# Kernel tuning notes

Measured on AMD Instinct MI355X. Metric: run time of the kernel, lower is better.

Reference implementation:

```python
import jax, jax.numpy as jnp
import numpy as np

# ASPPConv constants (from init_kwargs)
K = 9                      # kernel_size
DILATION = 6
PAD = DILATION * (K // 2)  # 24, 'same' padding for dilated conv
SIGMA = DILATION * 1.0     # self.sigma = dilation * sigma
BN_EPS = 1e-5


def setup_inputs() -> dict:
    key = jax.random.key(0)
    k1, k2, k3 = jax.random.split(key, 3)
    B, C, O, L = 8, 256, 16384, 0  # placeholder to keep names readable
    B, Cin, Cout, L = 8, 256, 256, 16384
    x = jax.random.normal(k1, (B, Cin, L), dtype=jnp.float32)
    coords = jax.random.uniform(k2, (B, 3, L), dtype=jnp.float32)  # xyz per point
    weight = jax.random.normal(k3, (Cout, Cin, K), dtype=jnp.float32) * 0.05
    gamma = jnp.ones((Cout,), jnp.float32)
    beta = jnp.zeros((Cout,), jnp.float32)
    return {"x": x, "coords": coords, "weight": weight, "gamma": gamma, "beta": beta}


def _weighted_conv1d(x, coords, weight):
    """Dilated conv1d where each tap is scaled by a Gaussian of the squared
    euclidean distance between the tap's coordinates and the center point's
    coordinates: w_k = exp(-||c_k - c_center||^2 / (2*sigma^2)).
    Zero padding (matches F.unfold) for both x and coords."""
    B, C, L = x.shape
    x_pad = jnp.pad(x, ((0, 0), (0, 0), (PAD, PAD)))
    c_pad = jnp.pad(coords, ((0, 0), (0, 0), (PAD, PAD)))
    inv_2s2 = 1.0 / (2.0 * SIGMA * SIGMA)
    out = jnp.zeros((B, weight.shape[0], L), x.dtype)
    # K=9 taps: small fixed loop; avoids materializing the [B,C,K,L] unfold.
    for k in range(K):
        off = k * DILATION
        xk = jax.lax.dynamic_slice_in_dim(x_pad, off, L, axis=2)   # [B,C,L]
        ck = jax.lax.dynamic_slice_in_dim(c_pad, off, L, axis=2)   # [B,3,L]
        dist2 = jnp.sum((ck - coords) ** 2, axis=1)                # [B,L]
        wk = jnp.exp(-dist2 * inv_2s2)                             # [B,L]
        out = out + jnp.einsum('bcl,oc->bol', xk * wk[:, None, :], weight[:, :, k])
    return out


def reference(x, coords, weight, gamma, beta):
    y = _weighted_conv1d(x, coords, weight)                        # [B,O,L]
    # BatchNorm1d (training mode): stats over batch and length per channel
    mean = jnp.mean(y, axis=(0, 2), keepdims=True)
    var = jnp.var(y, axis=(0, 2), keepdims=True)
    y = (y - mean) * jax.lax.rsqrt(var + BN_EPS)
    y = y * gamma[None, :, None] + beta[None, :, None]
    return jax.nn.relu(y)
```

## Files before the change

### kernel.cpp

```cpp
#include <hip/hip_runtime.h>
#include <hip/hip_bf16.h>

#define LEN   16384
#define CIN   256
#define COUT  256
#define NB    8
#define NTAP  9
#define DIL   6
#define PADW  24
#define NSTEP 72
#define PADROWS (LEN + 2*PADW)

typedef __bf16 bf16x8 __attribute__((ext_vector_type(8)));
typedef float  f32x4  __attribute__((ext_vector_type(4)));
typedef unsigned short u16;
typedef u16 u16x8 __attribute__((ext_vector_type(8)));

#define WKT_BYTES  (NB*NTAP*LEN*4)
#define WB_BYTES   (NSTEP*256*32*2)
#define XT_OFF     (WKT_BYTES + WB_BYTES)
#define XT_BYTES   ((size_t)NB*PADROWS*256*2)
#define SUMS_OFF   (XT_OFF + XT_BYTES)
#define SCB_OFF    (SUMS_OFF + 512*4)

#define GLOAD_LDS(g, l) __builtin_amdgcn_global_load_lds( \
    (const __attribute__((address_space(1))) void*)(g),   \
    (__attribute__((address_space(3))) void*)(l), 16, 0, 0)

__device__ __forceinline__ u16 f2bf(float v) {
    unsigned u = __builtin_bit_cast(unsigned, v);
    u += 0x7FFFu + ((u >> 16) & 1u);
    return (u16)(u >> 16);
}

__global__ __launch_bounds__(256) void k_wk(const float* __restrict__ coords,
                                            float* __restrict__ wkt) {
    int i = blockIdx.x * 256 + threadIdx.x;
    if (i >= NB * NTAP * LEN) return;
    int l = i & (LEN - 1);
    int bk = i >> 14;
    int k = bk % NTAP, b = bk / NTAP;
    const float* cb = coords + (size_t)b * 3 * LEN;
    int lt = l + k * DIL - PADW;
    bool ok = (unsigned)lt < (unsigned)LEN;
    float d2 = 0.f;
#pragma unroll
    for (int j = 0; j < 3; ++j) {
        float cc = cb[j * LEN + l];
        float ct = ok ? cb[j * LEN + lt] : 0.f;
        float d = ct - cc;
        d2 += d * d;
    }
    wkt[i] = expf(-d2 * (1.f / 72.f));
}

__global__ __launch_bounds__(256) void k_wb(const float* __restrict__ W,
                                            u16* __restrict__ Wb) {
    int i = blockIdx.x * 256 + threadIdx.x;
    if (i >= NSTEP * 256 * 32) return;
    int j = i & 31;
    int o = (i >> 5) & 255;
    int s = i >> 13;
    int k = s >> 3;
    int c = ((s & 7) << 5) + j;
    Wb[i] = f2bf(W[((size_t)o * CIN + c) * NTAP + k]);
}

__global__ __launch_bounds__(256) void k_xt(const float* __restrict__ x,
                                            u16* __restrict__ xt) {
    __shared__ float t[64 * 65];
    const int tid = threadIdx.x;
    const int cg  = blockIdx.x;
    const int rg  = blockIdx.y;
    const int b   = blockIdx.z;
    const int lx0 = rg * 64 - PADW;
#pragma unroll
    for (int i = 0; i < 4; ++i) {
        int c  = i * 16 + (tid >> 4);
        int l4 = (tid & 15) * 4;
        int lx = lx0 + l4;
        f32x4 v = {};
        if (lx >= 0 && lx + 3 < LEN)
            v = *reinterpret_cast<const f32x4*>(
                x + ((size_t)b * CIN + cg * 64 + c) * LEN + lx);
        float* tr = &t[c * 65 + l4];
        tr[0] = v[0]; tr[1] = v[1]; tr[2] = v[2]; tr[3] = v[3];
    }
    __syncthreads();
#pragma unroll
    for (int m = 0; m < 2; ++m) {
        int l    = m * 32 + (tid >> 3);
        int c0   = (tid & 7) * 8;
        int prow = rg * 64 + l;
        if (prow < PADROWS) {
            u16x8 o;
#pragma unroll
            for (int j = 0; j < 8; ++j) o[j] = f2bf(t[(c0 + j) * 65 + l]);
            *reinterpret_cast<u16x8*>(
                xt + ((size_t)b * PADROWS + prow) * 256 + cg * 64 + c0) = o;
        }
    }
}

__global__ __launch_bounds__(256, 2) void k_conv(
    const u16*   __restrict__ xt,
    const float* __restrict__ wkt,
    const u16*   __restrict__ Wb,
    float* __restrict__ y,
    float* __restrict__ sums)
{
    const int lt = blockIdx.x;
    const int ob = blockIdx.y;
    const int b  = blockIdx.z;
    const int l0 = lt * 128;
    const int tid  = threadIdx.x;
    const int lane = tid & 63;
    const int wid  = tid >> 6;
    const int wr = wid >> 1;
    const int wc = wid & 1;

    __shared__ u16 As[3][4096];
    __shared__ u16 Bs[3][4096];
    __shared__ float wkl[NTAP * 128];

    for (int i = tid; i < NTAP * 128; i += 256) {
        int k = i >> 7, l = i & 127;
        wkl[i] = wkt[((size_t)b * NTAP + k) * LEN + l0 + l];
    }

    f32x4 acc_f[4][4] = {};
    f32x4 acc_t[4][4] = {};

    const u16* wbBase = Wb + (size_t)ob * 4096;
    const u16* xtBase = xt + (size_t)b * PADROWS * 256;
    const int srcswz = ((lane & 3) ^ ((lane >> 3) & 3)) * 8;
    const int rsub   = lane >> 2;

    auto stage = [&](int bufi, int s) {
        const int ktap  = s >> 3;
        const int cbase = (s & 7) << 5;
#pragma unroll
        for (int j = 0; j < 2; ++j) {
            const int q = wid * 2 + j;
            const u16* ga = wbBase + (size_t)s * 8192 + (q * 16 + rsub) * 32 + srcswz;
            GLOAD_LDS(ga, &As[bufi][q * 512]);
            const u16* gb = xtBase
                + (size_t)(l0 + q * 16 + rsub + 6 * ktap) * 256
                + cbase + srcswz;
            GLOAD_LDS(gb, &Bs[bufi][q * 512]);
        }
    };

    stage(0, 0);
    stage(1, 1);
    __syncthreads();

    const int fr  = lane & 15;
    const int rdoff = fr * 32 + (((lane >> 4) ^ ((fr >> 1) & 3)) * 8);
    const int col = lane & 15;
    const int rg  = lane >> 4;

    for (int s = 0; s < NSTEP; ++s) {
        const int cur = s % 3;
        asm volatile("s_waitcnt vmcnt(4)" ::: "memory");
        __builtin_amdgcn_s_barrier();
        if (s + 2 < NSTEP) stage((s + 2) % 3, s + 2);

        bf16x8 af[4], bfv[4];
        const u16* Ab = &As[cur][wr * 2048 + rdoff];
        const u16* Bb = &Bs[cur][wc * 2048 + rdoff];
#pragma unroll
        for (int mi = 0; mi < 4; ++mi)
            af[mi] = *reinterpret_cast<const bf16x8*>(Ab + mi * 512);
#pragma unroll
        for (int ni = 0; ni < 4; ++ni)
            bfv[ni] = *reinterpret_cast<const bf16x8*>(Bb + ni * 512);
#pragma unroll
        for (int mi = 0; mi < 4; ++mi)
#pragma unroll
            for (int ni = 0; ni < 4; ++ni)
                acc_t[mi][ni] = __builtin_amdgcn_mfma_f32_16x16x32_bf16(
                    af[mi], bfv[ni], acc_t[mi][ni], 0, 0, 0);
        if ((s & 7) == 7) {
            const int ktap = s >> 3;
            float wv[4];
#pragma unroll
            for (int ni = 0; ni < 4; ++ni)
                wv[ni] = wkl[ktap * 128 + wc * 64 + ni * 16 + col];
#pragma unroll
            for (int mi = 0; mi < 4; ++mi)
#pragma unroll
                for (int ni = 0; ni < 4; ++ni) {
#pragma unroll
                    for (int r = 0; r < 4; ++r)
                        acc_f[mi][ni][r] += wv[ni] * acc_t[mi][ni][r];
                    acc_t[mi][ni] = f32x4{};
                }
        }
    }

    float* yb = y + ((size_t)b * COUT + ob * 128 + wr * 64) * LEN + l0 + wc * 64;
#pragma unroll
    for (int mi = 0; mi < 4; ++mi) {
#pragma unroll
        for (int r = 0; r < 4; ++r) {
            const int o_loc = mi * 16 + rg * 4 + r;
            float s1 = 0.f, s2 = 0.f;
#pragma unroll
            for (int ni = 0; ni < 4; ++ni) {
                float v = acc_f[mi][ni][r];
                yb[(size_t)o_loc * LEN + ni * 16 + col] = v;
                s1 += v;
                s2 += v * v;
            }
#pragma unroll
            for (int m = 1; m < 16; m <<= 1) {
                s1 += __shfl_xor(s1, m, 64);
                s2 += __shfl_xor(s2, m, 64);
            }
            if (col == 0) {
                int o = ob * 128 + wr * 64 + o_loc;
                atomicAdd(&sums[o], s1);
                atomicAdd(&sums[COUT + o], s2);
            }
        }
    }
}

__global__ __launch_bounds__(256) void k_stats(const float* __restrict__ sums,
                                               const float* __restrict__ gamma,
                                               const float* __restrict__ beta,
                                               float* __restrict__ scb) {
    int o = threadIdx.x;
    const float inv_n = 1.f / (float)(NB * LEN);
    float mean = sums[o] * inv_n;
    float var  = sums[COUT + o] * inv_n - mean * mean;
    float sc = gamma[o] * rsqrtf(var + 1e-5f);
    scb[o]        = sc;
    scb[COUT + o] = beta[o] - mean * sc;
}

__global__ __launch_bounds__(256) void k_norm(float* __restrict__ y,
                                              const float* __restrict__ scb) {
    const int total4 = NB * COUT * LEN / 4;
    int i = blockIdx.x * 256 + threadIdx.x;
    for (; i < total4; i += gridDim.x * 256) {
        f32x4 v = reinterpret_cast<f32x4*>(y)[i];
        int o = (i >> 12) & 255;
        float sc = scb[o], bi = scb[COUT + o];
#pragma unroll
        for (int j = 0; j < 4; ++j)
            v[j] = fmaxf(v[j] * sc + bi, 0.f);
        reinterpret_cast<f32x4*>(y)[i] = v;
    }
}

extern "C" void kernel_launch(void* const* d_in, const int* in_sizes, int n_in,
                              void* d_out, int out_size, void* d_ws, size_t ws_size,
                              hipStream_t stream) {
    const float* x      = (const float*)d_in[0];
    const float* coords = (const float*)d_in[1];
    const float* W      = (const float*)d_in[2];
    const float* gamma  = (const float*)d_in[3];
    const float* beta   = (const float*)d_in[4];
    float* out = (float*)d_out;
    char*  ws  = (char*)d_ws;

    float* wkt  = (float*)ws;
    u16*   Wb   = (u16*)(ws + WKT_BYTES);
    u16*   xtp  = (u16*)(ws + XT_OFF);
    float* sums = (float*)(ws + SUMS_OFF);
    float* scb  = (float*)(ws + SCB_OFF);

    hipMemsetAsync(sums, 0, 512 * 4, stream);

    k_wk<<<(NB * NTAP * LEN + 255) / 256, 256, 0, stream>>>(coords, wkt);
    k_wb<<<(NSTEP * 256 * 32 + 255) / 256, 256, 0, stream>>>(W, Wb);
    k_xt<<<dim3(4, (PADROWS + 63) / 64, NB), 256, 0, stream>>>(x, xtp);

    dim3 g(LEN / 128, 2, NB);
    k_conv<<<g, 256, 0, stream>>>(xtp, wkt, Wb, out, sums);

    k_stats<<<1, 256, 0, stream>>>(sums, gamma, beta, scb);
    k_norm<<<2048, 256, 0, stream>>>(out, scb);
}
```

Baseline: 441.7 us.

## Deepen LDS pipeline to 4 buffers and double-buffer register fragments around MFMA

Moves the shared-memory ring from 3 to 4 stages with three loads in flight, and unrolls the k-loop by two. LDS fragment reads for the next step are ping-ponged into a second register set so they overlap the current step's MFMAs. MFMA blocks are wrapped in s_setprio to favour matrix issue across waves. This raises LDS use and register pressure and adds barriers, which may reduce occupancy at two blocks per CU.

```diff
diff --git a/kernel.cpp b/kernel.cpp
--- a/kernel.cpp
+++ b/kernel.cpp
@@ -119,8 +119,8 @@
     const int wr = wid >> 1;
     const int wc = wid & 1;
 
-    __shared__ u16 As[3][4096];
-    __shared__ u16 Bs[3][4096];
+    __shared__ u16 As[4][4096];
+    __shared__ u16 Bs[4][4096];
     __shared__ float wkl[NTAP * 128];
 
     for (int i = tid; i < NTAP * 128; i += 256) {
@@ -136,7 +136,8 @@
     const int srcswz = ((lane & 3) ^ ((lane >> 3) & 3)) * 8;
     const int rsub   = lane >> 2;
 
-    auto stage = [&](int bufi, int s) {
+    auto stage = [&](int s) {
+        const int bufi  = s & 3;
         const int ktap  = s >> 3;
         const int cbase = (s & 7) << 5;
 #pragma unroll
@@ -151,52 +152,74 @@
         }
     };
 
-    stage(0, 0);
-    stage(1, 1);
-    __syncthreads();
-
-    const int fr  = lane & 15;
+    const int fr    = lane & 15;
     const int rdoff = fr * 32 + (((lane >> 4) ^ ((fr >> 1) & 3)) * 8);
-    const int col = lane & 15;
-    const int rg  = lane >> 4;
-
-    for (int s = 0; s < NSTEP; ++s) {
-        const int cur = s % 3;
-        asm volatile("s_waitcnt vmcnt(4)" ::: "memory");
-        __builtin_amdgcn_s_barrier();
-        if (s + 2 < NSTEP) stage((s + 2) % 3, s + 2);
-
-        bf16x8 af[4], bfv[4];
-        const u16* Ab = &As[cur][wr * 2048 + rdoff];
-        const u16* Bb = &Bs[cur][wc * 2048 + rdoff];
+    const int col   = lane & 15;
+    const int rg    = lane >> 4;
+
+    auto readf = [&](bf16x8* af, bf16x8* bfv, int s) {
+        const u16* Ab = &As[s & 3][wr * 2048 + rdoff];
+        const u16* Bb = &Bs[s & 3][wc * 2048 + rdoff];
 #pragma unroll
         for (int mi = 0; mi < 4; ++mi)
             af[mi] = *reinterpret_cast<const bf16x8*>(Ab + mi * 512);
 #pragma unroll
         for (int ni = 0; ni < 4; ++ni)
             bfv[ni] = *reinterpret_cast<const bf16x8*>(Bb + ni * 512);
+    };
+
+    auto domfma = [&](bf16x8* af, bf16x8* bfv) {
+        __builtin_amdgcn_s_setprio(1);
 #pragma unroll
         for (int mi = 0; mi < 4; ++mi)
 #pragma unroll
             for (int ni = 0; ni < 4; ++ni)
                 acc_t[mi][ni] = __builtin_amdgcn_mfma_f32_16x16x32_bf16(
                     af[mi], bfv[ni], acc_t[mi][ni], 0, 0, 0);
-        if ((s & 7) == 7) {
-            const int ktap = s >> 3;
-            float wv[4];
-#pragma unroll
-            for (int ni = 0; ni < 4; ++ni)
-                wv[ni] = wkl[ktap * 128 + wc * 64 + ni * 16 + col];
-#pragma unroll
-            for (int mi = 0; mi < 4; ++mi)
-#pragma unroll
-                for (int ni = 0; ni < 4; ++ni) {
-#pragma unroll
-                    for (int r = 0; r < 4; ++r)
-                        acc_f[mi][ni][r] += wv[ni] * acc_t[mi][ni][r];
-                    acc_t[mi][ni] = f32x4{};
-                }
-        }
+        __builtin_amdgcn_s_setprio(0);
+    };
+
+    auto fold = [&](int s) {
+        const int ktap = s >> 3;
+        float wv[4];
+#pragma unroll
+        for (int ni = 0; ni < 4; ++ni)
+            wv[ni] = wkl[ktap * 128 + wc * 64 + ni * 16 + col];
+#pragma unroll
+        for (int mi = 0; mi < 4; ++mi)
+#pragma unroll
+            for (int ni = 0; ni < 4; ++ni) {
+#pragma unroll
+                for (int r = 0; r < 4; ++r)
+                    acc_f[mi][ni][r] += wv[ni] * acc_t[mi][ni][r];
+                acc_t[mi][ni] = f32x4{};
+            }
+    };
+
+    bf16x8 afA[4], bfA[4], afB[4], bfB[4];
+
+    stage(0); stage(1); stage(2);
+    asm volatile("s_waitcnt vmcnt(4)" ::: "memory");
+    __builtin_amdgcn_s_barrier();
+    readf(afA, bfA, 0);
+
+    for (int t = 0; t < 36; ++t) {
+        const int s0 = 2 * t;
+        const int s1 = 2 * t + 1;
+        readf(afB, bfB, s0 + 1);
+        if (t <= 34) stage(s0 + 3);
+        if (t < 35) asm volatile("s_waitcnt vmcnt(4)" ::: "memory");
+        __builtin_amdgcn_s_barrier();
+        domfma(afA, bfA);
+        __builtin_amdgcn_s_barrier();
+        if (t < 35) readf(afA, bfA, s1 + 1);
+        if (t <= 33) stage(s1 + 3);
+        if (t < 34) asm volatile("s_waitcnt vmcnt(4)" ::: "memory");
+        else if (t == 34) asm volatile("s_waitcnt vmcnt(0)" ::: "memory");
+        __builtin_amdgcn_s_barrier();
+        domfma(afB, bfB);
+        if ((t & 3) == 3) fold(s1);
+        __builtin_amdgcn_s_barrier();
     }
 
     float* yb = y + ((size_t)b * COUT + ob * 128 + wr * 64) * LEN + l0 + wc * 64;
```

Result: faster. 378.3 us (-14.4%).

## Load conv B operand directly to registers, drop LDS staging, swizzle block order

Applied to the files above, without the earlier changes.

The conv kernel no longer stages the activation (B) tiles through shared memory. Each wave loads its bf16 fragments straight from global memory into double-buffered registers, while the weight (A) tiles still go through a triple-buffered LDS ring. The per-tap Gaussian weights are read from global memory at fold time instead of being preloaded into LDS. The grid is flattened and remapped so that consecutive blocks spread across batch and output halves, and MFMA sections get raised wave priority. This cuts LDS traffic and footprint, possibly allowing more occupancy, at the cost of uncoalesced, redundant global loads and more registers.

```diff
diff --git a/kernel.cpp b/kernel.cpp
--- a/kernel.cpp
+++ b/kernel.cpp
@@ -109,9 +109,10 @@
     float* __restrict__ y,
     float* __restrict__ sums)
 {
-    const int lt = blockIdx.x;
-    const int ob = blockIdx.y;
-    const int b  = blockIdx.z;
+    const int swz = (blockIdx.x & 7) * 256 + (blockIdx.x >> 3);
+    const int lt = swz & 127;
+    const int ob = (swz >> 7) & 1;
+    const int b  = swz >> 8;
     const int l0 = lt * 128;
     const int tid  = threadIdx.x;
     const int lane = tid & 63;
@@ -120,83 +121,101 @@
     const int wc = wid & 1;
 
     __shared__ u16 As[3][4096];
-    __shared__ u16 Bs[3][4096];
-    __shared__ float wkl[NTAP * 128];
-
-    for (int i = tid; i < NTAP * 128; i += 256) {
-        int k = i >> 7, l = i & 127;
-        wkl[i] = wkt[((size_t)b * NTAP + k) * LEN + l0 + l];
-    }
 
     f32x4 acc_f[4][4] = {};
     f32x4 acc_t[4][4] = {};
 
     const u16* wbBase = Wb + (size_t)ob * 4096;
-    const u16* xtBase = xt + (size_t)b * PADROWS * 256;
     const int srcswz = ((lane & 3) ^ ((lane >> 3) & 3)) * 8;
-    const int rsub   = lane >> 2;
-
-    auto stage = [&](int bufi, int s) {
-        const int ktap  = s >> 3;
-        const int cbase = (s & 7) << 5;
+
+    auto stageA = [&](int s) {
+        const int slot = s % 3;
 #pragma unroll
         for (int j = 0; j < 2; ++j) {
-            const int q = wid * 2 + j;
-            const u16* ga = wbBase + (size_t)s * 8192 + (q * 16 + rsub) * 32 + srcswz;
-            GLOAD_LDS(ga, &As[bufi][q * 512]);
-            const u16* gb = xtBase
-                + (size_t)(l0 + q * 16 + rsub + 6 * ktap) * 256
-                + cbase + srcswz;
-            GLOAD_LDS(gb, &Bs[bufi][q * 512]);
+            const int r = j * 64 + wid * 16 + (lane >> 2);
+            const u16* ga = wbBase + (size_t)s * 8192 + r * 32 + srcswz;
+            GLOAD_LDS(ga, &As[slot][j * 2048 + wid * 512]);
         }
     };
 
-    stage(0, 0);
-    stage(1, 1);
-    __syncthreads();
-
     const int fr  = lane & 15;
+    const int kg8 = (lane >> 4) * 8;
     const int rdoff = fr * 32 + (((lane >> 4) ^ ((fr >> 1) & 3)) * 8);
     const int col = lane & 15;
     const int rg  = lane >> 4;
 
-    for (int s = 0; s < NSTEP; ++s) {
-        const int cur = s % 3;
-        asm volatile("s_waitcnt vmcnt(4)" ::: "memory");
-        __builtin_amdgcn_s_barrier();
-        if (s + 2 < NSTEP) stage((s + 2) % 3, s + 2);
-
-        bf16x8 af[4], bfv[4];
-        const u16* Ab = &As[cur][wr * 2048 + rdoff];
-        const u16* Bb = &Bs[cur][wc * 2048 + rdoff];
+    const u16* xw = xt + ((size_t)b * PADROWS + l0 + wc * 64 + fr) * 256 + kg8;
+    const float* wkp = wkt + (size_t)b * NTAP * LEN + l0 + wc * 64 + col;
+
+    auto loadB = [&](bf16x8* bank, int s) {
+        const int tap = s >> 3, cc = s & 7;
+        const u16* bp = xw + tap * (DIL * 256) + cc * 32;
+#pragma unroll
+        for (int ni = 0; ni < 4; ++ni)
+            bank[ni] = *reinterpret_cast<const bf16x8*>(bp + ni * 16 * 256);
+    };
+
+    bf16x8 afr[4];
+    auto readA = [&](int s) {
+        const u16* Ab = &As[s % 3][wr * 2048 + rdoff];
 #pragma unroll
         for (int mi = 0; mi < 4; ++mi)
-            af[mi] = *reinterpret_cast<const bf16x8*>(Ab + mi * 512);
-#pragma unroll
-        for (int ni = 0; ni < 4; ++ni)
-            bfv[ni] = *reinterpret_cast<const bf16x8*>(Bb + ni * 512);
+            afr[mi] = *reinterpret_cast<const bf16x8*>(Ab + mi * 512);
+    };
+
+    auto domfma = [&](bf16x8* bank) {
+        __builtin_amdgcn_s_setprio(1);
 #pragma unroll
         for (int mi = 0; mi < 4; ++mi)
 #pragma unroll
             for (int ni = 0; ni < 4; ++ni)
                 acc_t[mi][ni] = __builtin_amdgcn_mfma_f32_16x16x32_bf16(
-                    af[mi], bfv[ni], acc_t[mi][ni], 0, 0, 0);
-        if ((s & 7) == 7) {
-            const int ktap = s >> 3;
-            float wv[4];
-#pragma unroll
-            for (int ni = 0; ni < 4; ++ni)
-                wv[ni] = wkl[ktap * 128 + wc * 64 + ni * 16 + col];
-#pragma unroll
-            for (int mi = 0; mi < 4; ++mi)
-#pragma unroll
-                for (int ni = 0; ni < 4; ++ni) {
-#pragma unroll
-                    for (int r = 0; r < 4; ++r)
-                        acc_f[mi][ni][r] += wv[ni] * acc_t[mi][ni][r];
-                    acc_t[mi][ni] = f32x4{};
-                }
-        }
+                    afr[mi], bank[ni], acc_t[mi][ni], 0, 0, 0);
+        __builtin_amdgcn_s_setprio(0);
+    };
+
+    auto fold = [&](int s) {
+        const int tap = s >> 3;
+        float wv[4];
+#pragma unroll
+        for (int ni = 0; ni < 4; ++ni)
+            wv[ni] = wkp[(size_t)tap * LEN + ni * 16];
+#pragma unroll
+        for (int mi = 0; mi < 4; ++mi)
+#pragma unroll
+            for (int ni = 0; ni < 4; ++ni) {
+#pragma unroll
+                for (int r = 0; r < 4; ++r)
+                    acc_f[mi][ni][r] += wv[ni] * acc_t[mi][ni][r];
+                acc_t[mi][ni] = f32x4{};
+            }
+    };
+
+    bf16x8 B0[4], B1[4];
+
+    stageA(0); stageA(1);
+    loadB(B0, 0);
+
+    for (int t = 0; t < 36; ++t) {
+        const int s0 = 2 * t;
+        const int s1 = 2 * t + 1;
+        loadB(B1, s0 + 1);
+        asm volatile("s_waitcnt vmcnt(6)" ::: "memory");
+        __builtin_amdgcn_s_barrier();
+        asm volatile("" ::: "memory");
+        if (s0 + 2 < NSTEP) stageA(s0 + 2);
+        readA(s0);
+        domfma(B0);
+        if ((s0 & 7) == 7) fold(s0);
+        if (s1 + 1 < NSTEP) loadB(B0, s1 + 1);
+        if (t < 35) asm volatile("s_waitcnt vmcnt(6)" ::: "memory");
+        else        asm volatile("s_waitcnt vmcnt(0)" ::: "memory");
+        __builtin_amdgcn_s_barrier();
+        asm volatile("" ::: "memory");
+        if (s1 + 2 < NSTEP) stageA(s1 + 2);
+        readA(s1);
+        domfma(B1);
+        if ((s1 & 7) == 7) fold(s1);
     }
 
     float* yb = y + ((size_t)b * COUT + ob * 128 + wr * 64) * LEN + l0 + wc * 64;
@@ -278,8 +297,7 @@
     k_wb<<<(NSTEP * 256 * 32 + 255) / 256, 256, 0, stream>>>(W, Wb);
     k_xt<<<dim3(4, (PADROWS + 63) / 64, NB), 256, 0, stream>>>(x, xtp);
 
-    dim3 g(LEN / 128, 2, NB);
-    k_conv<<<g, 256, 0, stream>>>(xtp, wkt, Wb, out, sums);
+    k_conv<<<2048, 256, 0, stream>>>(xtp, wkt, Wb, out, sums);
 
     k_stats<<<1, 256, 0, stream>>>(sums, gamma, beta, scb);
     k_norm<<<2048, 256, 0, stream>>>(out, scb);
```

Result: slower. 634.6 us (+43.7%).

## Raise conv occupancy, swizzle block order, drop wk LDS staging, add MFMA priority

Applied to the files above, without the earlier changes.

The conv kernel moves to a 1D grid with an XCD-style block swizzle, so blocks that share batch and weight data are grouped. Launch bounds go from 2 to 3 blocks per SM to allow more waves in flight. The per-block LDS copy of the Gaussian tap weights and its initial __syncthreads are removed; the weights are instead read straight from global memory at each tap boundary. The MFMA section is wrapped in s_setprio, ring slots are tracked incrementally, and the final step drains with vmcnt(0). The cost is possible register spills under the tighter launch bound and scattered global loads in the tap epilogue.

```diff
diff --git a/kernel.cpp b/kernel.cpp
--- a/kernel.cpp
+++ b/kernel.cpp
@@ -102,16 +102,17 @@
     }
 }
 
-__global__ __launch_bounds__(256, 2) void k_conv(
+__global__ __launch_bounds__(256, 3) void k_conv(
     const u16*   __restrict__ xt,
     const float* __restrict__ wkt,
     const u16*   __restrict__ Wb,
     float* __restrict__ y,
     float* __restrict__ sums)
 {
-    const int lt = blockIdx.x;
-    const int ob = blockIdx.y;
-    const int b  = blockIdx.z;
+    const int swz = (blockIdx.x & 7) * 256 + (blockIdx.x >> 3);
+    const int lt = swz & 127;
+    const int ob = (swz >> 7) & 1;
+    const int b  = swz >> 8;
     const int l0 = lt * 128;
     const int tid  = threadIdx.x;
     const int lane = tid & 63;
@@ -121,12 +122,6 @@
 
     __shared__ u16 As[3][4096];
     __shared__ u16 Bs[3][4096];
-    __shared__ float wkl[NTAP * 128];
-
-    for (int i = tid; i < NTAP * 128; i += 256) {
-        int k = i >> 7, l = i & 127;
-        wkl[i] = wkt[((size_t)b * NTAP + k) * LEN + l0 + l];
-    }
 
     f32x4 acc_f[4][4] = {};
     f32x4 acc_t[4][4] = {};
@@ -136,57 +131,63 @@
     const int srcswz = ((lane & 3) ^ ((lane >> 3) & 3)) * 8;
     const int rsub   = lane >> 2;
 
-    auto stage = [&](int bufi, int s) {
+    auto stage = [&](int slot, int s) {
         const int ktap  = s >> 3;
         const int cbase = (s & 7) << 5;
 #pragma unroll
         for (int j = 0; j < 2; ++j) {
             const int q = wid * 2 + j;
             const u16* ga = wbBase + (size_t)s * 8192 + (q * 16 + rsub) * 32 + srcswz;
-            GLOAD_LDS(ga, &As[bufi][q * 512]);
+            GLOAD_LDS(ga, &As[slot][q * 512]);
             const u16* gb = xtBase
                 + (size_t)(l0 + q * 16 + rsub + 6 * ktap) * 256
                 + cbase + srcswz;
-            GLOAD_LDS(gb, &Bs[bufi][q * 512]);
+            GLOAD_LDS(gb, &Bs[slot][q * 512]);
         }
     };
+
+    const int fr    = lane & 15;
+    const int rdoff = fr * 32 + (((lane >> 4) ^ ((fr >> 1) & 3)) * 8);
+    const int col   = lane & 15;
+    const int rg    = lane >> 4;
+
+    const float* wkp = wkt + (size_t)b * NTAP * LEN + l0 + wc * 64 + col;
 
     stage(0, 0);
     stage(1, 1);
-    __syncthreads();
-
-    const int fr  = lane & 15;
-    const int rdoff = fr * 32 + (((lane >> 4) ^ ((fr >> 1) & 3)) * 8);
-    const int col = lane & 15;
-    const int rg  = lane >> 4;
-
+
+    int rslot = 0, wslot = 2;
     for (int s = 0; s < NSTEP; ++s) {
-        const int cur = s % 3;
-        asm volatile("s_waitcnt vmcnt(4)" ::: "memory");
-        __builtin_amdgcn_s_barrier();
-        if (s + 2 < NSTEP) stage((s + 2) % 3, s + 2);
-
-        bf16x8 af[4], bfv[4];
-        const u16* Ab = &As[cur][wr * 2048 + rdoff];
-        const u16* Bb = &Bs[cur][wc * 2048 + rdoff];
+        if (s < NSTEP - 1) asm volatile("s_waitcnt vmcnt(4)" ::: "memory");
+        else               asm volatile("s_waitcnt vmcnt(0)" ::: "memory");
+        asm volatile("s_barrier" ::: "memory");
+        if (s + 2 < NSTEP) stage(wslot, s + 2);
+
+        bf16x8 afr[4], bfr[4];
+        const u16* Ab = &As[rslot][wr * 2048 + rdoff];
+        const u16* Bb = &Bs[rslot][wc * 2048 + rdoff];
 #pragma unroll
         for (int mi = 0; mi < 4; ++mi)
-            af[mi] = *reinterpret_cast<const bf16x8*>(Ab + mi * 512);
+            afr[mi] = *reinterpret_cast<const bf16x8*>(Ab + mi * 512);
 #pragma unroll
         for (int ni = 0; ni < 4; ++ni)
-            bfv[ni] = *reinterpret_cast<const bf16x8*>(Bb + ni * 512);
+            bfr[ni] = *reinterpret_cast<const bf16x8*>(Bb + ni * 512);
+
+        __builtin_amdgcn_s_setprio(1);
 #pragma unroll
         for (int mi = 0; mi < 4; ++mi)
 #pragma unroll
             for (int ni = 0; ni < 4; ++ni)
                 acc_t[mi][ni] = __builtin_amdgcn_mfma_f32_16x16x32_bf16(
-                    af[mi], bfv[ni], acc_t[mi][ni], 0, 0, 0);
+                    afr[mi], bfr[ni], acc_t[mi][ni], 0, 0, 0);
+        __builtin_amdgcn_s_setprio(0);
+
         if ((s & 7) == 7) {
-            const int ktap = s >> 3;
+            const int tap = s >> 3;
             float wv[4];
 #pragma unroll
             for (int ni = 0; ni < 4; ++ni)
-                wv[ni] = wkl[ktap * 128 + wc * 64 + ni * 16 + col];
+                wv[ni] = wkp[(size_t)tap * LEN + ni * 16];
 #pragma unroll
             for (int mi = 0; mi < 4; ++mi)
 #pragma unroll
@@ -197,6 +198,8 @@
                     acc_t[mi][ni] = f32x4{};
                 }
         }
+        rslot = (rslot == 2) ? 0 : rslot + 1;
+        wslot = (wslot == 2) ? 0 : wslot + 1;
     }
 
     float* yb = y + ((size_t)b * COUT + ob * 128 + wr * 64) * LEN + l0 + wc * 64;
@@ -278,8 +281,7 @@
     k_wb<<<(NSTEP * 256 * 32 + 255) / 256, 256, 0, stream>>>(W, Wb);
     k_xt<<<dim3(4, (PADROWS + 63) / 64, NB), 256, 0, stream>>>(x, xtp);
 
-    dim3 g(LEN / 128, 2, NB);
-    k_conv<<<g, 256, 0, stream>>>(xtp, wkt, Wb, out, sums);
+    k_conv<<<2048, 256, 0, stream>>>(xtp, wkt, Wb, out, sums);
 
     k_stats<<<1, 256, 0, stream>>>(sums, gamma, beta, scb);
     k_norm<<<2048, 256, 0, stream>>>(out, scb);
```

After: 605.8 us. 37.1% more time.
